# Kernel tuning notes

Measured on AMD Instinct MI355X. Metric: run time of the kernel, lower is better.

The kernel has to match this reference:

```python
import jax, jax.numpy as jnp
import numpy as np

IN_CH = 128
HID = 256   # 2 * out_channels
OUT_CH = 128
N_NODES = 10000
N_EDGES = 640000


def setup_inputs() -> dict:
    key = jax.random.key(0)
    ks = jax.random.split(key, 6)
    x = jax.random.normal(ks[0], (N_NODES, IN_CH), dtype=jnp.float32)
    edge_index = jax.random.randint(ks[1], (2, N_EDGES), 0, N_NODES, dtype=jnp.int64)
    # GCNConv params (glorot-like scale)
    W1 = jax.random.normal(ks[2], (IN_CH, HID), dtype=jnp.float32) / np.sqrt(IN_CH)
    b1 = jnp.zeros((HID,), dtype=jnp.float32)
    W2 = jax.random.normal(ks[3], (HID, OUT_CH), dtype=jnp.float32) / np.sqrt(HID)
    b2 = jnp.zeros((OUT_CH,), dtype=jnp.float32)
    return {"x": x, "edge_index": edge_index, "W1": W1, "b1": b1, "W2": W2, "b2": b2}


def _gcn_norm(edge_index, n_nodes):
    """Add self-loops and compute symmetric GCN normalization per edge."""
    loops = jnp.arange(n_nodes, dtype=edge_index.dtype)
    src = jnp.concatenate([edge_index[0], loops])  # [E+N]
    dst = jnp.concatenate([edge_index[1], loops])
    deg = jax.ops.segment_sum(jnp.ones_like(dst, dtype=jnp.float32), dst,
                              num_segments=n_nodes)
    dinv = jnp.where(deg > 0, jax.lax.rsqrt(deg), 0.0)
    norm = dinv[src] * dinv[dst]  # [E+N]
    return src, dst, norm


def _gcn_layer(x, W, b, src, dst, norm, n_nodes):
    h = x @ W                                  # [N, F_out]
    msg = h[src] * norm[:, None]               # gather + scale, [E+N, F_out]
    agg = jax.ops.segment_sum(msg, dst, num_segments=n_nodes)
    return agg + b


def reference(x, edge_index, W1, b1, W2, b2):
    n = x.shape[0]
    src, dst, norm = _gcn_norm(edge_index, n)
    h = jax.nn.relu(_gcn_layer(x, W1, b1, src, dst, norm, n))
    out = jax.nn.relu(_gcn_layer(h, W2, b2, src, dst, norm, n))
    return out
```

## Files before the change

kernel.cpp:

```cpp
#include <hip/hip_runtime.h>

#define N_FEAT 128
#define HID 256
#define OUT_CH 128

#define NB 256
#define MAXN 10240
#define CH 16
#define CB (NB / CH)

__device__ __forceinline__ unsigned bf16rn(float f) {
    unsigned u = __float_as_uint(f);
    return (u + 0x7fffu + ((u >> 16) & 1u)) >> 16;
}
__device__ __forceinline__ unsigned pack_bf16x2(float lo, float hi) {
    return bf16rn(lo) | (bf16rn(hi) << 16);
}
__device__ __forceinline__ float2 unpack_bf16x2(unsigned u) {
    float2 r;
    r.x = __uint_as_float(u << 16);
    r.y = __uint_as_float(u & 0xffff0000u);
    return r;
}


__global__ __launch_bounds__(256)
void hist_kernel(const int* __restrict__ dst, unsigned short* __restrict__ bh,
                 int E, int N, int chunk) {
    __shared__ int hist[MAXN];
    for (int i = threadIdx.x; i < N; i += 256) hist[i] = 0;
    __syncthreads();
    int base = blockIdx.x * chunk;
    int lim = min(chunk, E - base);
    for (int i = threadIdx.x; i < lim; i += 256) {
        int d = dst[base + i];
        if (d >= 0 && d < N) atomicAdd(&hist[d], 1);
    }
    __syncthreads();
    unsigned short* out = bh + (size_t)blockIdx.x * N;
    for (int i = threadIdx.x; i < N; i += 256) out[i] = (unsigned short)hist[i];
}

__global__ __launch_bounds__(256)
void colsum_kernel(const unsigned short* __restrict__ bh,
                   int* __restrict__ ps, int N) {
    int j = blockIdx.x * 256 + threadIdx.x;
    if (j >= N) return;
    int c = blockIdx.y;
    int s = 0;
    #pragma unroll
    for (int b = c * CB; b < (c + 1) * CB; b++) s += bh[(size_t)b * N + j];
    ps[(size_t)c * N + j] = s;
}

__global__ __launch_bounds__(256)
void colscan_kernel(int* __restrict__ ps, int* __restrict__ counts,
                    float* __restrict__ dinv, int N) {
    int j = blockIdx.x * 256 + threadIdx.x;
    if (j >= N) return;
    int run = 0;
    #pragma unroll
    for (int c = 0; c < CH; c++) {
        size_t idx = (size_t)c * N + j;
        int t = ps[idx];
        ps[idx] = run;
        run += t;
    }
    counts[j] = run;
    dinv[j] = rsqrtf((float)(run + 1));
}

#define SCAN_T 1024
#define SCAN_MAX_PER 16
__global__ __launch_bounds__(SCAN_T)
void scan_kernel(const int* __restrict__ counts,
                 int* __restrict__ row_start, int n) {
    int tid = threadIdx.x;
    int per = (n + SCAN_T - 1) / SCAN_T;
    int base = tid * per;
    int local[SCAN_MAX_PER];
    int sum = 0;
    for (int j = 0; j < per; j++) {
        int i = base + j;
        int c = (i < n) ? counts[i] : 0;
        local[j] = sum;
        sum += c;
    }
    int lane = tid & 63;
    int wave = tid >> 6;
    int incl = sum;
    #pragma unroll
    for (int off = 1; off < 64; off <<= 1) {
        int t = __shfl_up(incl, off, 64);
        if (lane >= off) incl += t;
    }
    __shared__ int wsum[16];
    __shared__ int woff[16];
    if (lane == 63) wsum[wave] = incl;
    __syncthreads();
    if (wave == 0) {
        int w = (lane < 16) ? wsum[lane] : 0;
        int v = w;
        #pragma unroll
        for (int off = 1; off < 16; off <<= 1) {
            int t = __shfl_up(v, off, 64);
            if (lane >= off) v += t;
        }
        if (lane < 16) woff[lane] = v - w;
    }
    __syncthreads();
    int thread_excl = woff[wave] + (incl - sum);
    for (int j = 0; j < per; j++) {
        int i = base + j;
        if (i < n) row_start[i] = thread_excl + local[j];
    }
    if (tid == SCAN_T - 1) row_start[n] = thread_excl + sum;
}

__global__ __launch_bounds__(256)
void chunkbase_kernel(unsigned short* __restrict__ bh,
                      const int* __restrict__ ps, int N) {
    int j = blockIdx.x * 256 + threadIdx.x;
    if (j >= N) return;
    int c = blockIdx.y;
    int run = ps[(size_t)c * N + j];
    #pragma unroll
    for (int b = c * CB; b < (c + 1) * CB; b++) {
        size_t idx = (size_t)b * N + j;
        int t = bh[idx];
        bh[idx] = (unsigned short)run;
        run += t;
    }
}

__global__ __launch_bounds__(256)
void scat_kernel(const int* __restrict__ src, const int* __restrict__ dst,
                 const unsigned short* __restrict__ bh,
                 const int* __restrict__ row_start,
                 int* __restrict__ csr_src, int E, int N, int chunk) {
    __shared__ int cur[MAXN];
    const unsigned short* basep = bh + (size_t)blockIdx.x * N;
    for (int i = threadIdx.x; i < N; i += 256)
        cur[i] = row_start[i] + (int)basep[i];
    __syncthreads();
    int base = blockIdx.x * chunk;
    int lim = min(chunk, E - base);
    for (int i = threadIdx.x; i < lim; i += 256) {
        int e = base + i;
        int d = dst[e];
        if (d < 0 || d >= N) continue;
        int pos = atomicAdd(&cur[d], 1);
        if ((unsigned)pos < (unsigned)E) csr_src[pos] = src[e];
    }
}

__global__ void prescale_kernel(const float* __restrict__ x,
                                const float* __restrict__ dinv,
                                unsigned* __restrict__ xs_b, int total4) {
    int i = blockIdx.x * blockDim.x + threadIdx.x;
    if (i < total4) {
        int row = i >> 5;
        float d = dinv[row];
        float4 v = ((const float4*)x)[i];
        uint2 p;
        p.x = pack_bf16x2(v.x * d, v.y * d);
        p.y = pack_bf16x2(v.z * d, v.w * d);
        ((uint2*)xs_b)[i] = p;
    }
}

template <bool EPILOGUE>
__global__ __launch_bounds__(256)
void agg_kernel(const unsigned* __restrict__ featb,
                const float* __restrict__ dinv,
                const int* __restrict__ row_start,
                const int* __restrict__ csr_src,
                const float* __restrict__ bias,
                float* __restrict__ out, int N) {
    int wave = threadIdx.x >> 6;
    int n = blockIdx.x * 4 + wave;
    if (n >= N) return;
    int f = threadIdx.x & 63;
    float dn = dinv[n];
    float2 v = unpack_bf16x2(featb[(size_t)n * 64 + f]);
    float accx = v.x;
    float accy = v.y;
    int e0 = row_start[n];
    int e1 = row_start[n + 1];
    int e = e0;
    for (; e + 16 <= e1; e += 16) {
        int s[16];
        #pragma unroll
        for (int j = 0; j < 16; j++) s[j] = csr_src[e + j];
        unsigned w[16];
        #pragma unroll
        for (int j = 0; j < 16; j++) w[j] = featb[(size_t)s[j] * 64 + f];
        #pragma unroll
        for (int j = 0; j < 16; j++) {
            float2 u = unpack_bf16x2(w[j]);
            accx += u.x;
            accy += u.y;
        }
    }
    for (; e + 4 <= e1; e += 4) {
        int s0 = csr_src[e], s1 = csr_src[e + 1];
        int s2 = csr_src[e + 2], s3 = csr_src[e + 3];
        unsigned w0 = featb[(size_t)s0 * 64 + f];
        unsigned w1 = featb[(size_t)s1 * 64 + f];
        unsigned w2 = featb[(size_t)s2 * 64 + f];
        unsigned w3 = featb[(size_t)s3 * 64 + f];
        float2 u0 = unpack_bf16x2(w0), u1 = unpack_bf16x2(w1);
        float2 u2 = unpack_bf16x2(w2), u3 = unpack_bf16x2(w3);
        accx += u0.x + u1.x + u2.x + u3.x;
        accy += u0.y + u1.y + u2.y + u3.y;
    }
    for (; e < e1; ++e) {
        float2 u = unpack_bf16x2(featb[(size_t)csr_src[e] * 64 + f]);
        accx += u.x;
        accy += u.y;
    }
    accx *= dn;
    accy *= dn;
    if (EPILOGUE) {
        float2 b = ((const float2*)bias)[f];
        accx = fmaxf(accx + b.x, 0.0f);
        accy = fmaxf(accy + b.y, 0.0f);
    }
    float2 r;
    r.x = accx;
    r.y = accy;
    ((float2*)out)[(size_t)n * 64 + f] = r;
}

template <bool BIAS_RELU, bool RSCALE, bool BF16_OUT>
__global__ __launch_bounds__(256)
void gemm_kernel(const float* __restrict__ A,
                 const float* __restrict__ B,
                 const float* __restrict__ bias,
                 const float* __restrict__ rscale,
                 void* __restrict__ Cv, int M, int N, int K) {
    __shared__ float As[16][68];
    __shared__ float Bs[16][64];
    int tid = threadIdx.x;
    int n0 = blockIdx.x * 64;
    int m0 = blockIdx.y * 64;
    int tx = tid & 15;
    int ty = tid >> 4;
    int ar = tid >> 2;
    int akq = tid & 3;
    int bk = tid >> 4;
    int bnq = tid & 15;
    float acc[4][4] = {};
    for (int k0 = 0; k0 < K; k0 += 16) {
        float4 av = make_float4(0.f, 0.f, 0.f, 0.f);
        if (m0 + ar < M)
            av = *(const float4*)&A[(size_t)(m0 + ar) * K + k0 + akq * 4];
        float4 bv = *(const float4*)&B[(size_t)(k0 + bk) * N + n0 + bnq * 4];
        As[akq * 4 + 0][ar] = av.x;
        As[akq * 4 + 1][ar] = av.y;
        As[akq * 4 + 2][ar] = av.z;
        As[akq * 4 + 3][ar] = av.w;
        *(float4*)&Bs[bk][bnq * 4] = bv;
        __syncthreads();
        #pragma unroll
        for (int k = 0; k < 16; k++) {
            float4 ra = *(const float4*)&As[k][ty * 4];
            float4 rb = *(const float4*)&Bs[k][tx * 4];
            acc[0][0] = fmaf(ra.x, rb.x, acc[0][0]);
            acc[0][1] = fmaf(ra.x, rb.y, acc[0][1]);
            acc[0][2] = fmaf(ra.x, rb.z, acc[0][2]);
            acc[0][3] = fmaf(ra.x, rb.w, acc[0][3]);
            acc[1][0] = fmaf(ra.y, rb.x, acc[1][0]);
            acc[1][1] = fmaf(ra.y, rb.y, acc[1][1]);
            acc[1][2] = fmaf(ra.y, rb.z, acc[1][2]);
            acc[1][3] = fmaf(ra.y, rb.w, acc[1][3]);
            acc[2][0] = fmaf(ra.z, rb.x, acc[2][0]);
            acc[2][1] = fmaf(ra.z, rb.y, acc[2][1]);
            acc[2][2] = fmaf(ra.z, rb.z, acc[2][2]);
            acc[2][3] = fmaf(ra.z, rb.w, acc[2][3]);
            acc[3][0] = fmaf(ra.w, rb.x, acc[3][0]);
            acc[3][1] = fmaf(ra.w, rb.y, acc[3][1]);
            acc[3][2] = fmaf(ra.w, rb.z, acc[3][2]);
            acc[3][3] = fmaf(ra.w, rb.w, acc[3][3]);
        }
        __syncthreads();
    }
    #pragma unroll
    for (int i = 0; i < 4; i++) {
        int m = m0 + ty * 4 + i;
        if (m >= M) continue;
        float rs = RSCALE ? rscale[m] : 1.0f;
        float v[4];
        #pragma unroll
        for (int j = 0; j < 4; j++) {
            v[j] = acc[i][j];
            if (RSCALE) v[j] *= rs;
            if (BIAS_RELU) v[j] = fmaxf(v[j] + bias[n0 + tx * 4 + j], 0.0f);
        }
        if (BF16_OUT) {
            unsigned* Cb = (unsigned*)Cv;
            size_t base = (size_t)m * (N >> 1) + ((n0 + tx * 4) >> 1);
            Cb[base] = pack_bf16x2(v[0], v[1]);
            Cb[base + 1] = pack_bf16x2(v[2], v[3]);
        } else {
            float* C = (float*)Cv;
            #pragma unroll
            for (int j = 0; j < 4; j++)
                C[(size_t)m * N + n0 + tx * 4 + j] = v[j];
        }
    }
}


static inline size_t align512(size_t x) { return (x + 511) & ~(size_t)511; }

extern "C" void kernel_launch(void* const* d_in, const int* in_sizes, int n_in,
                              void* d_out, int out_size, void* d_ws, size_t ws_size,
                              hipStream_t stream) {
    const float* x = (const float*)d_in[0];
    const int* ei = (const int*)d_in[1];
    const float* W1 = (const float*)d_in[2];
    const float* b1 = (const float*)d_in[3];
    const float* W2 = (const float*)d_in[4];
    const float* b2 = (const float*)d_in[5];
    float* out = (float*)d_out;

    const int N = in_sizes[0] / N_FEAT;
    const int E = in_sizes[1] / 2;
    const int* src = ei;
    const int* dst = ei + E;

    char* ws = (char*)d_ws;
    size_t off = 0;
    float* dinv = (float*)(ws + off);    off += align512((size_t)N * 4);
    int* counts = (int*)(ws + off);      off += align512((size_t)N * 4);
    int* row_start = (int*)(ws + off);   off += align512((size_t)(N + 1) * 4);
    int* csr_src = (int*)(ws + off);     off += align512((size_t)E * 4);
    unsigned* xs_b = (unsigned*)(ws + off); off += align512((size_t)N * 64 * 4);
    float* h = (float*)(ws + off);       off += align512((size_t)N * HID * 4);
    unsigned* t_b = (unsigned*)(ws + off); off += align512((size_t)N * 64 * 4);
    int* ps = (int*)(ws + off);          off += align512((size_t)CH * N * 4);
    unsigned short* bh = (unsigned short*)(ws + off);
    off += align512((size_t)NB * N * 2);
    (void)ws_size;
    float* agg1 = out;
    const int chunk = (E + NB - 1) / NB;
    const int NJ = (N + 255) / 256;

    hist_kernel<<<NB, 256, 0, stream>>>(dst, bh, E, N, chunk);
    colsum_kernel<<<dim3(NJ, CH), 256, 0, stream>>>(bh, ps, N);
    colscan_kernel<<<NJ, 256, 0, stream>>>(ps, counts, dinv, N);
    scan_kernel<<<1, SCAN_T, 0, stream>>>(counts, row_start, N);
    chunkbase_kernel<<<dim3(NJ, CH), 256, 0, stream>>>(bh, ps, N);
    scat_kernel<<<NB, 256, 0, stream>>>(src, dst, bh, row_start, csr_src, E, N, chunk);

    {
        int total4 = N * N_FEAT / 4;
        prescale_kernel<<<(total4 + 255) / 256, 256, 0, stream>>>(x, dinv, xs_b, total4);
    }

    agg_kernel<false><<<(N + 3) / 4, 256, 0, stream>>>(xs_b, dinv, row_start, csr_src,
                                                       nullptr, agg1, N);

    {
        dim3 grid(HID / 64, (N + 63) / 64);
        gemm_kernel<true, false, false><<<grid, 256, 0, stream>>>(
            agg1, W1, b1, nullptr, h, N, HID, N_FEAT);
    }

    {
        dim3 grid(OUT_CH / 64, (N + 63) / 64);
        gemm_kernel<false, true, true><<<grid, 256, 0, stream>>>(
            h, W2, nullptr, dinv, t_b, N, OUT_CH, HID);
    }

    agg_kernel<true><<<(N + 3) / 4, 256, 0, stream>>>(t_b, dinv, row_start, csr_src,
                                                      b2, out, N);
}
```

Baseline: 178.5 us.

## Merge colsum into colscan, process four nodes per wave, double GEMM k-tile

Folds the column-sum pass into the column-scan kernel so one launch both sums histogram chunks and writes exclusive prefixes. It also doubles the number of histogram blocks to 512. The aggregation kernel now has each wave loop over four consecutive nodes, with a quarter as many blocks, to cut launch and block overhead. The GEMM k-tile is doubled to 32 to halve the barrier count. The trade-offs are less parallelism in aggregation and colscan, a larger histogram buffer to read, and more shared memory per GEMM block.

```diff
diff --git a/kernel.cpp b/kernel.cpp
--- a/kernel.cpp
+++ b/kernel.cpp
@@ -4,7 +4,7 @@
 #define HID 256
 #define OUT_CH 128
 
-#define NB 256
+#define NB 512
 #define MAXN 10240
 #define CH 16
 #define CB (NB / CH)
@@ -42,29 +42,18 @@
 }
 
 __global__ __launch_bounds__(256)
-void colsum_kernel(const unsigned short* __restrict__ bh,
-                   int* __restrict__ ps, int N) {
-    int j = blockIdx.x * 256 + threadIdx.x;
-    if (j >= N) return;
-    int c = blockIdx.y;
-    int s = 0;
-    #pragma unroll
-    for (int b = c * CB; b < (c + 1) * CB; b++) s += bh[(size_t)b * N + j];
-    ps[(size_t)c * N + j] = s;
-}
-
-__global__ __launch_bounds__(256)
-void colscan_kernel(int* __restrict__ ps, int* __restrict__ counts,
+void colscan_kernel(const unsigned short* __restrict__ bh,
+                    int* __restrict__ ps, int* __restrict__ counts,
                     float* __restrict__ dinv, int N) {
     int j = blockIdx.x * 256 + threadIdx.x;
     if (j >= N) return;
     int run = 0;
-    #pragma unroll
     for (int c = 0; c < CH; c++) {
-        size_t idx = (size_t)c * N + j;
-        int t = ps[idx];
-        ps[idx] = run;
-        run += t;
+        int s = 0;
+        #pragma unroll
+        for (int b = c * CB; b < (c + 1) * CB; b++) s += bh[(size_t)b * N + j];
+        ps[(size_t)c * N + j] = run;
+        run += s;
     }
     counts[j] = run;
     dinv[j] = rsqrtf((float)(run + 1));
@@ -177,59 +166,60 @@
                 const int* __restrict__ csr_src,
                 const float* __restrict__ bias,
                 float* __restrict__ out, int N) {
-    int wave = threadIdx.x >> 6;
-    int n = blockIdx.x * 4 + wave;
-    if (n >= N) return;
+    int gw = blockIdx.x * 4 + (threadIdx.x >> 6);
     int f = threadIdx.x & 63;
-    float dn = dinv[n];
-    float2 v = unpack_bf16x2(featb[(size_t)n * 64 + f]);
-    float accx = v.x;
-    float accy = v.y;
-    int e0 = row_start[n];
-    int e1 = row_start[n + 1];
-    int e = e0;
-    for (; e + 16 <= e1; e += 16) {
-        int s[16];
-        #pragma unroll
-        for (int j = 0; j < 16; j++) s[j] = csr_src[e + j];
-        unsigned w[16];
-        #pragma unroll
-        for (int j = 0; j < 16; j++) w[j] = featb[(size_t)s[j] * 64 + f];
-        #pragma unroll
-        for (int j = 0; j < 16; j++) {
-            float2 u = unpack_bf16x2(w[j]);
+    int nEnd = min(gw * 4 + 4, N);
+    for (int n = gw * 4; n < nEnd; n++) {
+        float dn = dinv[n];
+        float2 v = unpack_bf16x2(featb[(size_t)n * 64 + f]);
+        float accx = v.x;
+        float accy = v.y;
+        int e0 = row_start[n];
+        int e1 = row_start[n + 1];
+        int e = e0;
+        for (; e + 16 <= e1; e += 16) {
+            int s[16];
+            #pragma unroll
+            for (int j = 0; j < 16; j++) s[j] = csr_src[e + j];
+            unsigned w[16];
+            #pragma unroll
+            for (int j = 0; j < 16; j++) w[j] = featb[(size_t)s[j] * 64 + f];
+            #pragma unroll
+            for (int j = 0; j < 16; j++) {
+                float2 u = unpack_bf16x2(w[j]);
+                accx += u.x;
+                accy += u.y;
+            }
+        }
+        for (; e + 4 <= e1; e += 4) {
+            int s0 = csr_src[e], s1 = csr_src[e + 1];
+            int s2 = csr_src[e + 2], s3 = csr_src[e + 3];
+            unsigned w0 = featb[(size_t)s0 * 64 + f];
+            unsigned w1 = featb[(size_t)s1 * 64 + f];
+            unsigned w2 = featb[(size_t)s2 * 64 + f];
+            unsigned w3 = featb[(size_t)s3 * 64 + f];
+            float2 u0 = unpack_bf16x2(w0), u1 = unpack_bf16x2(w1);
+            float2 u2 = unpack_bf16x2(w2), u3 = unpack_bf16x2(w3);
+            accx += u0.x + u1.x + u2.x + u3.x;
+            accy += u0.y + u1.y + u2.y + u3.y;
+        }
+        for (; e < e1; ++e) {
+            float2 u = unpack_bf16x2(featb[(size_t)csr_src[e] * 64 + f]);
             accx += u.x;
             accy += u.y;
         }
-    }
-    for (; e + 4 <= e1; e += 4) {
-        int s0 = csr_src[e], s1 = csr_src[e + 1];
-        int s2 = csr_src[e + 2], s3 = csr_src[e + 3];
-        unsigned w0 = featb[(size_t)s0 * 64 + f];
-        unsigned w1 = featb[(size_t)s1 * 64 + f];
-        unsigned w2 = featb[(size_t)s2 * 64 + f];
-        unsigned w3 = featb[(size_t)s3 * 64 + f];
-        float2 u0 = unpack_bf16x2(w0), u1 = unpack_bf16x2(w1);
-        float2 u2 = unpack_bf16x2(w2), u3 = unpack_bf16x2(w3);
-        accx += u0.x + u1.x + u2.x + u3.x;
-        accy += u0.y + u1.y + u2.y + u3.y;
-    }
-    for (; e < e1; ++e) {
-        float2 u = unpack_bf16x2(featb[(size_t)csr_src[e] * 64 + f]);
-        accx += u.x;
-        accy += u.y;
-    }
-    accx *= dn;
-    accy *= dn;
-    if (EPILOGUE) {
-        float2 b = ((const float2*)bias)[f];
-        accx = fmaxf(accx + b.x, 0.0f);
-        accy = fmaxf(accy + b.y, 0.0f);
-    }
-    float2 r;
-    r.x = accx;
-    r.y = accy;
-    ((float2*)out)[(size_t)n * 64 + f] = r;
+        accx *= dn;
+        accy *= dn;
+        if (EPILOGUE) {
+            float2 b = ((const float2*)bias)[f];
+            accx = fmaxf(accx + b.x, 0.0f);
+            accy = fmaxf(accy + b.y, 0.0f);
+        }
+        float2 r;
+        r.x = accx;
+        r.y = accy;
+        ((float2*)out)[(size_t)n * 64 + f] = r;
+    }
 }
 
 template <bool BIAS_RELU, bool RSCALE, bool BF16_OUT>
@@ -239,8 +229,8 @@
                  const float* __restrict__ bias,
                  const float* __restrict__ rscale,
                  void* __restrict__ Cv, int M, int N, int K) {
-    __shared__ float As[16][68];
-    __shared__ float Bs[16][64];
+    __shared__ float As[32][68];
+    __shared__ float Bs[32][64];
     int tid = threadIdx.x;
     int n0 = blockIdx.x * 64;
     int m0 = blockIdx.y * 64;
@@ -251,19 +241,28 @@
     int bk = tid >> 4;
     int bnq = tid & 15;
     float acc[4][4] = {};
-    for (int k0 = 0; k0 < K; k0 += 16) {
-        float4 av = make_float4(0.f, 0.f, 0.f, 0.f);
-        if (m0 + ar < M)
-            av = *(const float4*)&A[(size_t)(m0 + ar) * K + k0 + akq * 4];
-        float4 bv = *(const float4*)&B[(size_t)(k0 + bk) * N + n0 + bnq * 4];
-        As[akq * 4 + 0][ar] = av.x;
-        As[akq * 4 + 1][ar] = av.y;
-        As[akq * 4 + 2][ar] = av.z;
-        As[akq * 4 + 3][ar] = av.w;
-        *(float4*)&Bs[bk][bnq * 4] = bv;
+    for (int k0 = 0; k0 < K; k0 += 32) {
+        float4 av0 = make_float4(0.f, 0.f, 0.f, 0.f);
+        float4 av1 = make_float4(0.f, 0.f, 0.f, 0.f);
+        if (m0 + ar < M) {
+            av0 = *(const float4*)&A[(size_t)(m0 + ar) * K + k0 + akq * 4];
+            av1 = *(const float4*)&A[(size_t)(m0 + ar) * K + k0 + 16 + akq * 4];
+        }
+        float4 bv0 = *(const float4*)&B[(size_t)(k0 + bk) * N + n0 + bnq * 4];
+        float4 bv1 = *(const float4*)&B[(size_t)(k0 + bk + 16) * N + n0 + bnq * 4];
+        As[akq * 4 + 0][ar] = av0.x;
+        As[akq * 4 + 1][ar] = av0.y;
+        As[akq * 4 + 2][ar] = av0.z;
+        As[akq * 4 + 3][ar] = av0.w;
+        As[akq * 4 + 16][ar] = av1.x;
+        As[akq * 4 + 17][ar] = av1.y;
+        As[akq * 4 + 18][ar] = av1.z;
+        As[akq * 4 + 19][ar] = av1.w;
+        *(float4*)&Bs[bk][bnq * 4] = bv0;
+        *(float4*)&Bs[bk + 16][bnq * 4] = bv1;
         __syncthreads();
         #pragma unroll
-        for (int k = 0; k < 16; k++) {
+        for (int k = 0; k < 32; k++) {
             float4 ra = *(const float4*)&As[k][ty * 4];
             float4 rb = *(const float4*)&Bs[k][tx * 4];
             acc[0][0] = fmaf(ra.x, rb.x, acc[0][0]);
@@ -346,10 +345,10 @@
     float* agg1 = out;
     const int chunk = (E + NB - 1) / NB;
     const int NJ = (N + 255) / 256;
+    const int AGG_BLOCKS = (N + 15) / 16;
 
     hist_kernel<<<NB, 256, 0, stream>>>(dst, bh, E, N, chunk);
-    colsum_kernel<<<dim3(NJ, CH), 256, 0, stream>>>(bh, ps, N);
-    colscan_kernel<<<NJ, 256, 0, stream>>>(ps, counts, dinv, N);
+    colscan_kernel<<<NJ, 256, 0, stream>>>(bh, ps, counts, dinv, N);
     scan_kernel<<<1, SCAN_T, 0, stream>>>(counts, row_start, N);
     chunkbase_kernel<<<dim3(NJ, CH), 256, 0, stream>>>(bh, ps, N);
     scat_kernel<<<NB, 256, 0, stream>>>(src, dst, bh, row_start, csr_src, E, N, chunk);
@@ -359,8 +358,8 @@
         prescale_kernel<<<(total4 + 255) / 256, 256, 0, stream>>>(x, dinv, xs_b, total4);
     }
 
-    agg_kernel<false><<<(N + 3) / 4, 256, 0, stream>>>(xs_b, dinv, row_start, csr_src,
-                                                       nullptr, agg1, N);
+    agg_kernel<false><<<AGG_BLOCKS, 256, 0, stream>>>(xs_b, dinv, row_start, csr_src,
+                                                      nullptr, agg1, N);
 
     {
         dim3 grid(HID / 64, (N + 63) / 64);
@@ -374,6 +373,6 @@
             h, W2, nullptr, dinv, t_b, N, OUT_CH, HID);
     }
 
-    agg_kernel<true><<<(N + 3) / 4, 256, 0, stream>>>(t_b, dinv, row_start, csr_src,
-                                                      b2, out, N);
-}
+    agg_kernel<true><<<AGG_BLOCKS, 256, 0, stream>>>(t_b, dinv, row_start, csr_src,
+                                                     b2, out, N);
+}
```

New measurement: 191.1 us. +7.0%, slower.
